# Kernel optimization log

Hardware: AMD Instinct MI355X
Metric: run time of the kernel (lower is better)

## Reference

```python
import jax, jax.numpy as jnp
import numpy as np

T, N, U, K, P = 4096, 256, 128, 32, 128


def setup_inputs() -> dict:
    key = jax.random.key(0)
    ks = jax.random.split(key, 8)
    input_sequence = jax.random.normal(ks[0], (T, U, K), jnp.float32)
    # Stable diagonal dynamics: |A| in (0.5, 0.99), random phase.
    r = jax.random.uniform(ks[1], (N, K), jnp.float32, 0.5, 0.99)
    theta = jax.random.uniform(ks[2], (N, K), jnp.float32, 0.0, np.pi)
    A_re = r * jnp.cos(theta)
    A_im = r * jnp.sin(theta)
    s_b = 1.0 / np.sqrt(U)
    s_c = 1.0 / np.sqrt(N)
    B_re = jax.random.normal(ks[3], (N, U), jnp.float32) * s_b
    B_im = jax.random.normal(ks[4], (N, U), jnp.float32) * s_b
    C_re = jax.random.normal(ks[5], (P, N), jnp.float32) * s_c
    C_im = jax.random.normal(ks[6], (P, N), jnp.float32) * s_c
    D = jax.random.normal(ks[7], (P, U), jnp.float32) * s_b
    return dict(input_sequence=input_sequence, A_re=A_re, A_im=A_im,
                B_re=B_re, B_im=B_im, C_re=C_re, C_im=C_im, D=D)


def _binary_op(elem_i, elem_j):
    # (a_i, s_i) o (a_j, s_j) = (a_i * a_j, a_j * s_i + s_j)
    a_i, s_i = elem_i
    a_j, s_j = elem_j
    return (a_i * a_j, a_j * s_i + s_j)


def reference(input_sequence, A_re, A_im, B_re, B_im, C_re, C_im, D):
    A = (A_re + 1j * A_im).astype(jnp.complex64)        # (N, K) diagonal
    Bm = (B_re + 1j * B_im).astype(jnp.complex64)        # (N, U)
    Cm = (C_re + 1j * C_im).astype(jnp.complex64)        # (P, N)
    x_c = input_sequence.astype(jnp.complex64)           # (T, U, K)
    # inputs_t = B @ x_t  -> (T, N, K)
    inputs = jnp.einsum('nu,tuk->tnk', Bm, x_c)
    systems = jnp.broadcast_to(A, (input_sequence.shape[0],) + A.shape)
    _, states = jax.lax.associative_scan(_binary_op, (systems, inputs))
    # out_t = C @ state_t -> (T, P, K)
    out = jnp.real(jnp.einsum('pn,tnk->tpk', Cm, states))
    Du = jnp.einsum('pu,tuk->tpk', D, input_sequence)    # 2D D branch
    return out + Du
```

## Files before the change

kernel.cpp:

```cpp
#include <hip/hip_runtime.h>
#include <hip/hip_bf16.h>

namespace {

constexpr int T = 4096, N = 256, U = 128, K = 32, P = 128;
constexpr int NK = N * K;
constexpr int CL = 16;
constexpr int NCH = T / CL;
constexpr int NG = NCH / 8;
constexpr int TB = 8;

typedef __attribute__((ext_vector_type(8))) short short8;
typedef __attribute__((ext_vector_type(4))) float f32x4;
typedef __attribute__((address_space(3))) unsigned lds_u32;
typedef __attribute__((address_space(1))) const unsigned glb_u32;

__device__ __forceinline__ unsigned short f2bf(float f) {
  union { float f; unsigned u; } v; v.f = f;
  unsigned r = v.u + 0x7FFFu + ((v.u >> 16) & 1u);
  return (unsigned short)(r >> 16);
}
__device__ __forceinline__ float bf2f(unsigned short s) {
  union { unsigned u; float f; } v; v.u = ((unsigned)s) << 16;
  return v.f;
}
__device__ __forceinline__ short8 ld8(const unsigned short* p) {
  return *reinterpret_cast<const short8*>(p);
}
__device__ __forceinline__ void dma16(const unsigned* g, unsigned* l) {
  __builtin_amdgcn_global_load_lds((glb_u32*)g, (lds_u32*)l, 16, 0, 0);
}
__device__ __forceinline__ void csq(float& pr, float& pi) {
  float nr = pr * pr - pi * pi, ni = 2.f * pr * pi; pr = nr; pi = ni;
}

__device__ __forceinline__ int zswz(int k, int n) {
  int n8 = n >> 3, j = n & 7;
  return k * 256 + ((n8 ^ (k & 7)) << 3) + (j ^ (((k >> 3) & 1) << 2));
}

__device__ __forceinline__ void unpackAB(uint4 a, uint4 b, short8& re, short8& im) {
  union { short8 v; unsigned u[4]; } r, i;
  r.u[0] = (a.x & 0xFFFFu) | (a.y << 16);
  i.u[0] = (a.x >> 16)     | (a.y & 0xFFFF0000u);
  r.u[1] = (a.z & 0xFFFFu) | (a.w << 16);
  i.u[1] = (a.z >> 16)     | (a.w & 0xFFFF0000u);
  r.u[2] = (b.x & 0xFFFFu) | (b.y << 16);
  i.u[2] = (b.x >> 16)     | (b.y & 0xFFFF0000u);
  r.u[3] = (b.z & 0xFFFFu) | (b.w << 16);
  i.u[3] = (b.z >> 16)     | (b.w & 0xFFFF0000u);
  re = r.v; im = i.v;
}

__global__ __launch_bounds__(256) void k_params(
    const float* Are, const float* Aim, const float* Bre, const float* Bim,
    const float* Cre, const float* Cim, const float* D,
    unsigned short* bre, unsigned short* bim, unsigned short* cre,
    unsigned short* cimn, unsigned short* dbf, float* atre, float* atim) {
  int idx = blockIdx.x * 256 + threadIdx.x;
  int stride = gridDim.x * 256;
  for (int i = idx; i < N * U; i += stride) { bre[i] = f2bf(Bre[i]); bim[i] = f2bf(Bim[i]); }
  for (int i = idx; i < P * N; i += stride) { cre[i] = f2bf(Cre[i]); cimn[i] = f2bf(-Cim[i]); }
  for (int i = idx; i < P * U; i += stride) { dbf[i] = f2bf(D[i]); }
  for (int i = idx; i < NK; i += stride) {
    int k = i >> 8, r = i & 255;
    int n8 = (r >> 3) ^ (k & 7);
    int j  = (r & 7) ^ (((k >> 3) & 1) << 2);
    int n = n8 * 8 + j;
    atre[i] = Are[n * K + k];
    atim[i] = Aim[n * K + k];
  }
}

__global__ __launch_bounds__(256) void k_castx(const float* x, unsigned* xTu) {
  __shared__ float lds[U * 33];
  int t = blockIdx.x, tid = threadIdx.x;
  const float* xt = x + (size_t)t * (U * K);
#pragma unroll
  for (int it = 0; it < 16; it++) {
    int idx = it * 256 + tid;
    int u = idx >> 5, k = idx & 31;
    lds[u * 33 + k] = xt[idx];
  }
  __syncthreads();
  unsigned* dst = xTu + (size_t)t * (K * U / 2);
#pragma unroll
  for (int it = 0; it < 8; it++) {
    int k = it * 4 + (tid >> 6);
    int up = tid & 63;
    float f0 = lds[(2 * up) * 33 + k];
    float f1 = lds[(2 * up + 1) * 33 + k];
    dst[k * 64 + up] = (unsigned)f2bf(f0) | ((unsigned)f2bf(f1) << 16);
  }
}

__global__ __launch_bounds__(256)
__attribute__((amdgpu_waves_per_eu(2, 2)))
void k_bgemm(const unsigned short* xT, const unsigned short* bre,
             const unsigned short* bim, unsigned* zbuf, int t0) {
  int blk = blockIdx.x, tid = threadIdx.x;
  int w = tid >> 6, l = tid & 63, lq = l >> 4, lr = l & 15;
  short8 Bf_re[4][4], Bf_im[4][4];
#pragma unroll
  for (int s = 0; s < 4; s++)
#pragma unroll
    for (int nt = 0; nt < 4; nt++) {
      int n0 = (w * 4 + nt) * 16;
      Bf_re[s][nt] = ld8(bre + (n0 + lr) * U + s * 32 + lq * 8);
      Bf_im[s][nt] = ld8(bim + (n0 + lr) * U + s * 32 + lq * 8);
    }
#pragma unroll
  for (int tl = 0; tl < TB; tl++) {
    int tloc = blk * TB + tl;
    const unsigned short* xrow = xT + (size_t)(t0 + tloc) * (K * U);
    short8 af[4][2];
#pragma unroll
    for (int s = 0; s < 4; s++) {
      af[s][0] = ld8(xrow + lr * U + s * 32 + lq * 8);
      af[s][1] = ld8(xrow + (16 + lr) * U + s * 32 + lq * 8);
    }
    f32x4 accre[2][4], accim[2][4];
#pragma unroll
    for (int a = 0; a < 2; a++)
#pragma unroll
      for (int b = 0; b < 4; b++) { accre[a][b] = (f32x4)0.f; accim[a][b] = (f32x4)0.f; }
#pragma unroll
    for (int s = 0; s < 4; s++)
#pragma unroll
      for (int nt = 0; nt < 4; nt++)
#pragma unroll
        for (int mt = 0; mt < 2; mt++) {
          accre[mt][nt] = __builtin_amdgcn_mfma_f32_16x16x32_bf16(af[s][mt], Bf_re[s][nt], accre[mt][nt], 0, 0, 0);
          accim[mt][nt] = __builtin_amdgcn_mfma_f32_16x16x32_bf16(af[s][mt], Bf_im[s][nt], accim[mt][nt], 0, 0, 0);
        }
    unsigned* dst = zbuf + (size_t)tloc * NK;
#pragma unroll
    for (int mt = 0; mt < 2; mt++)
#pragma unroll
      for (int nt = 0; nt < 4; nt++) {
        int n0 = (w * 4 + nt) * 16;
#pragma unroll
        for (int r = 0; r < 4; r++) {
          int krow = mt * 16 + lq * 4 + r;
          dst[zswz(krow, n0 + lr)] =
              (unsigned)f2bf(accre[mt][nt][r]) | ((unsigned)f2bf(accim[mt][nt][r]) << 16);
        }
      }
  }
}

__global__ __launch_bounds__(256) void k_scanA(const unsigned* zbuf, const float* atre,
                                               const float* atim, float2* cend, int c0) {
  int bid = blockIdx.x;
  int cl = bid >> 5;
  int lane = (bid & 31) * 256 + threadIdx.x;
  float ar = atre[lane], ai = atim[lane];
  float sr = 0.f, si = 0.f;
  const unsigned* src = zbuf + (size_t)cl * CL * NK + lane;
#pragma unroll 8
  for (int i = 0; i < CL; i++) {
    unsigned v = src[(size_t)i * NK];
    float ur = bf2f((unsigned short)(v & 0xFFFFu));
    float ui = bf2f((unsigned short)(v >> 16));
    float nr = ar * sr - ai * si + ur;
    float ni = ar * si + ai * sr + ui;
    sr = nr; si = ni;
  }
  cend[(size_t)(c0 + cl) * NK + lane] = make_float2(sr, si);
}

__global__ __launch_bounds__(256) void k_carryg(const float2* cend, const float* atre,
                                                const float* atim, float2* gagg) {
  int bid = blockIdx.x;
  int g = bid >> 5;
  int lane = (bid & 31) * 256 + threadIdx.x;
  float pr = atre[lane], pi = atim[lane];
#pragma unroll
  for (int i = 0; i < 4; i++) csq(pr, pi);
  float agr = 0.f, agi = 0.f;
#pragma unroll
  for (int j = 0; j < 8; j++) {
    float2 e = cend[(size_t)(g * 8 + j) * NK + lane];
    float nr = pr * agr - pi * agi + e.x;
    float ni = pr * agi + pi * agr + e.y;
    agr = nr; agi = ni;
  }
  gagg[(size_t)g * NK + lane] = make_float2(agr, agi);
}

__global__ __launch_bounds__(256) void k_carryb(float2* gagg, const float* atre,
                                                const float* atim) {
  int lane = blockIdx.x * 256 + threadIdx.x;
  float pr = atre[lane], pi = atim[lane];
#pragma unroll
  for (int i = 0; i < 7; i++) csq(pr, pi);
  float cr = 0.f, ci = 0.f;
  for (int gg = 0; gg < NG / 8; gg++) {
    float2 buf[8];
#pragma unroll
    for (int j = 0; j < 8; j++) buf[j] = gagg[(size_t)(gg * 8 + j) * NK + lane];
#pragma unroll
    for (int j = 0; j < 8; j++) {
      gagg[(size_t)(gg * 8 + j) * NK + lane] = make_float2(cr, ci);
      float nr = pr * cr - pi * ci + buf[j].x;
      float ni = pr * ci + pi * cr + buf[j].y;
      cr = nr; ci = ni;
    }
  }
}

__global__ __launch_bounds__(256) void k_carryf(float2* cend, const float* atre,
                                                const float* atim, const float2* gagg) {
  int bid = blockIdx.x;
  int g = bid >> 5;
  int lane = (bid & 31) * 256 + threadIdx.x;
  float pr = atre[lane], pi = atim[lane];
#pragma unroll
  for (int i = 0; i < 4; i++) csq(pr, pi);
  float2 c = gagg[(size_t)g * NK + lane];
  float cr = c.x, ci = c.y;
#pragma unroll
  for (int j = 0; j < 8; j++) {
    size_t off = (size_t)(g * 8 + j) * NK + lane;
    float2 e = cend[off];
    cend[off] = make_float2(cr, ci);
    float nr = pr * cr - pi * ci + e.x;
    float ni = pr * ci + pi * cr + e.y;
    cr = nr; ci = ni;
  }
}

__global__ __launch_bounds__(512)
__attribute__((amdgpu_waves_per_eu(2, 2)))
void k_scout(const unsigned* zbuf, const float* atre, const float* atim,
             const float2* cend,
             const unsigned short* cre, const unsigned short* cimn,
             const unsigned short* dbf, const unsigned short* xT,
             float* out, int t0, int gc0) {
  __shared__ unsigned ldsz[3][NK];
  int blk = blockIdx.x, tid = threadIdx.x;
  int w = tid >> 6, l = tid & 63, lq = l >> 4, lr = l & 15;
  int h = (lr >> 3) & 1;
  short8 Cf_re[8], Cf_im[8];
#pragma unroll
  for (int s = 0; s < 8; s++) {
    int p = w * 16 + lr;
    Cf_re[s] = ld8(cre  + p * N + s * 32 + lq * 8);
    Cf_im[s] = ld8(cimn + p * N + s * 32 + lq * 8);
  }
  short8 Df[4];
#pragma unroll
  for (int s = 0; s < 4; s++) {
    int p = w * 16 + lr;
    Df[s] = ld8(dbf + p * U + s * 32 + lq * 8);
  }
  float ar[16], ai[16], sr[16], si[16];
  int gc = gc0 + blk;
#pragma unroll
  for (int it = 0; it < 4; it++)
#pragma unroll
    for (int j = 0; j < 4; j++) {
      int idx = it * 2048 + tid * 4 + j;
      int e = it * 4 + j;
      ar[e] = atre[idx]; ai[e] = atim[idx];
      float2 c0 = cend[(size_t)gc * NK + idx];
      sr[e] = c0.x; si[e] = c0.y;
    }
  const unsigned* zch = zbuf + (size_t)(blk * CL) * NK;
#pragma unroll
  for (int it = 0; it < 4; it++)
    dma16(zch + it * 2048 + tid * 4, &ldsz[0][it * 2048 + tid * 4]);
#pragma unroll
  for (int it = 0; it < 4; it++)
    dma16(zch + NK + it * 2048 + tid * 4, &ldsz[1][it * 2048 + tid * 4]);

  int bc = 0;
  for (int tl = 0; tl < CL; tl++) {
    int t = t0 + blk * CL + tl;
    const unsigned short* xt = xT + (size_t)t * (K * U);
    short8 xfr[4][2];
#pragma unroll
    for (int s = 0; s < 4; s++)
#pragma unroll
      for (int kt = 0; kt < 2; kt++)
        xfr[s][kt] = ld8(xt + (kt * 16 + lr) * U + s * 32 + lq * 8);
    if (tl == 0) { asm volatile("s_waitcnt vmcnt(12)" ::: "memory"); }
    else         { asm volatile("s_waitcnt vmcnt(20)" ::: "memory"); }
    unsigned* zl = &ldsz[bc][0];
#pragma unroll
    for (int it = 0; it < 4; it++) {
      unsigned* p4 = zl + it * 2048 + tid * 4;
      uint4 v = *reinterpret_cast<const uint4*>(p4);
      unsigned d0 = v.x, d1 = v.y, d2 = v.z, d3 = v.w;
#pragma unroll
      for (int j = 0; j < 4; j++) {
        unsigned dv = (j == 0) ? d0 : (j == 1) ? d1 : (j == 2) ? d2 : d3;
        int e = it * 4 + j;
        float ur = bf2f((unsigned short)(dv & 0xFFFFu));
        float ui = bf2f((unsigned short)(dv >> 16));
        float nr = ar[e] * sr[e] - ai[e] * si[e] + ur;
        float ni = ar[e] * si[e] + ai[e] * sr[e] + ui;
        sr[e] = nr; si[e] = ni;
        dv = (unsigned)f2bf(nr) | ((unsigned)f2bf(ni) << 16);
        if (j == 0) d0 = dv; else if (j == 1) d1 = dv; else if (j == 2) d2 = dv; else d3 = dv;
      }
      uint4 o; o.x = d0; o.y = d1; o.z = d2; o.w = d3;
      *reinterpret_cast<uint4*>(p4) = o;
    }
    asm volatile("s_waitcnt lgkmcnt(0)" ::: "memory");
    __builtin_amdgcn_s_barrier();
    __builtin_amdgcn_sched_barrier(0);
    if (tl + 2 < CL) {
      int bn = bc + 2; if (bn >= 3) bn -= 3;
      const unsigned* zn = zbuf + (size_t)(blk * CL + tl + 2) * NK;
#pragma unroll
      for (int it = 0; it < 4; it++)
        dma16(zn + it * 2048 + tid * 4, &ldsz[bn][it * 2048 + tid * 4]);
    }
    f32x4 acc[2];
    acc[0] = (f32x4)0.f; acc[1] = (f32x4)0.f;
    const unsigned* zs = &ldsz[bc][0];
#pragma unroll
    for (int s = 0; s < 8; s++) {
      short8 bfr[2], bfi[2];
#pragma unroll
      for (int kt = 0; kt < 2; kt++) {
        int k = kt * 16 + lr;
        int n8 = s * 4 + lq;
        const uint4* qp = reinterpret_cast<const uint4*>(zs + k * 256 + ((n8 ^ (k & 7)) << 3));
        uint4 a = qp[h], b = qp[h ^ 1];
        unpackAB(a, b, bfr[kt], bfi[kt]);
      }
#pragma unroll
      for (int kt = 0; kt < 2; kt++) {
        acc[kt] = __builtin_amdgcn_mfma_f32_16x16x32_bf16(Cf_re[s], bfr[kt], acc[kt], 0, 0, 0);
        acc[kt] = __builtin_amdgcn_mfma_f32_16x16x32_bf16(Cf_im[s], bfi[kt], acc[kt], 0, 0, 0);
      }
    }
#pragma unroll
    for (int s = 0; s < 4; s++)
#pragma unroll
      for (int kt = 0; kt < 2; kt++)
        acc[kt] = __builtin_amdgcn_mfma_f32_16x16x32_bf16(Df[s], xfr[s][kt], acc[kt], 0, 0, 0);
    float* ot = out + (size_t)t * (P * K);
#pragma unroll
    for (int kt = 0; kt < 2; kt++)
#pragma unroll
      for (int r = 0; r < 4; r++) {
        int p = w * 16 + lq * 4 + r;
        int k = kt * 16 + lr;
        ot[p * K + k] = acc[kt][r];
      }
    bc = bc + 1; if (bc >= 3) bc -= 3;
  }
}

}

extern "C" void kernel_launch(void* const* d_in, const int* in_sizes, int n_in,
                              void* d_out, int out_size, void* d_ws, size_t ws_size,
                              hipStream_t stream) {
  const float* x   = (const float*)d_in[0];
  const float* Are = (const float*)d_in[1];
  const float* Aim = (const float*)d_in[2];
  const float* Bre = (const float*)d_in[3];
  const float* Bim = (const float*)d_in[4];
  const float* Cre = (const float*)d_in[5];
  const float* Cim = (const float*)d_in[6];
  const float* D   = (const float*)d_in[7];
  float* out = (float*)d_out;

  auto al = [](size_t x_) { return (x_ + 255) & ~(size_t)255; };
  const size_t fixed = al((size_t)T * K * U * 2)
                     + al((size_t)NCH * NK * 8)
                     + al((size_t)NG * NK * 8)
                     + 2 * al((size_t)N * U * 2)
                     + 2 * al((size_t)P * N * 2)
                     + al((size_t)P * U * 2)
                     + 2 * al((size_t)NK * 4);
  int S = 64;
  for (int s : {1, 2, 4, 8, 16, 32, 64}) {
    if (fixed + al((size_t)(T / s) * NK * 4) <= ws_size) { S = s; break; }
  }
  const int TS = T / S;
  const int CS = NCH / S;

  char* w = (char*)d_ws;
  auto alloc = [&](size_t bytes) { void* p = (void*)w; w += (bytes + 255) & ~(size_t)255; return p; };
  unsigned* zbuf       = (unsigned*)alloc((size_t)TS * NK * 4);
  unsigned* xTu        = (unsigned*)alloc((size_t)T * K * U * 2);
  float2* cend         = (float2*)alloc((size_t)NCH * NK * 8);
  float2* gagg         = (float2*)alloc((size_t)NG * NK * 8);
  unsigned short* bre  = (unsigned short*)alloc((size_t)N * U * 2);
  unsigned short* bim  = (unsigned short*)alloc((size_t)N * U * 2);
  unsigned short* cre  = (unsigned short*)alloc((size_t)P * N * 2);
  unsigned short* cimn = (unsigned short*)alloc((size_t)P * N * 2);
  unsigned short* dbf  = (unsigned short*)alloc((size_t)P * U * 2);
  float* atre          = (float*)alloc((size_t)NK * 4);
  float* atim          = (float*)alloc((size_t)NK * 4);

  k_params<<<64, 256, 0, stream>>>(Are, Aim, Bre, Bim, Cre, Cim, D,
                                   bre, bim, cre, cimn, dbf, atre, atim);
  k_castx<<<T, 256, 0, stream>>>(x, xTu);

  const unsigned short* xT16 = (const unsigned short*)xTu;
  for (int q = 0; q < S; q++) {
    k_bgemm<<<TS / TB, 256, 0, stream>>>(xT16, bre, bim, zbuf, q * TS);
    k_scanA<<<CS * 32, 256, 0, stream>>>(zbuf, atre, atim, cend, q * CS);
  }
  k_carryg<<<NG * 32, 256, 0, stream>>>(cend, atre, atim, gagg);
  k_carryb<<<NK / 256, 256, 0, stream>>>(gagg, atre, atim);
  k_carryf<<<NG * 32, 256, 0, stream>>>(cend, atre, atim, gagg);
  for (int q = 0; q < S; q++) {
    if (S > 1)
      k_bgemm<<<TS / TB, 256, 0, stream>>>(xT16, bre, bim, zbuf, q * TS);
    k_scout<<<TS / CL, 512, 0, stream>>>(zbuf, atre, atim, cend,
                                         cre, cimn, dbf, xT16, out, q * TS, q * CS);
  }
}
```

Before: 265.8 us.

## Fuse chunk-local scan into B-GEMM kernel and drop separate scan pass

```diff
diff --git a/kernel.cpp b/kernel.cpp
--- a/kernel.cpp
+++ b/kernel.cpp
@@ -8,7 +8,7 @@
 constexpr int CL = 16;
 constexpr int NCH = T / CL;
 constexpr int NG = NCH / 8;
-constexpr int TB = 8;
+constexpr int TB = 16;
 
 typedef __attribute__((ext_vector_type(8))) short short8;
 typedef __attribute__((ext_vector_type(4))) float f32x4;
@@ -94,21 +94,36 @@
   }
 }
 
-__global__ __launch_bounds__(256)
+__global__ __launch_bounds__(512)
 __attribute__((amdgpu_waves_per_eu(2, 2)))
 void k_bgemm(const unsigned short* xT, const unsigned short* bre,
-             const unsigned short* bim, unsigned* zbuf, int t0) {
+             const unsigned short* bim, const float* atre, const float* atim,
+             unsigned* zbuf, float2* cend, int t0, int c0, int wr_cend) {
   int blk = blockIdx.x, tid = threadIdx.x;
   int w = tid >> 6, l = tid & 63, lq = l >> 4, lr = l & 15;
-  short8 Bf_re[4][4], Bf_im[4][4];
+  short8 Bf_re[4][2], Bf_im[4][2];
 #pragma unroll
   for (int s = 0; s < 4; s++)
 #pragma unroll
-    for (int nt = 0; nt < 4; nt++) {
-      int n0 = (w * 4 + nt) * 16;
+    for (int nt = 0; nt < 2; nt++) {
+      int n0 = (w * 2 + nt) * 16;
       Bf_re[s][nt] = ld8(bre + (n0 + lr) * U + s * 32 + lq * 8);
       Bf_im[s][nt] = ld8(bim + (n0 + lr) * U + s * 32 + lq * 8);
     }
+  float ar[16], ai[16], sr[16], si[16];
+#pragma unroll
+  for (int mt = 0; mt < 2; mt++)
+#pragma unroll
+    for (int nt = 0; nt < 2; nt++)
+#pragma unroll
+      for (int r = 0; r < 4; r++) {
+        int e = mt * 8 + nt * 4 + r;
+        int krow = mt * 16 + lq * 4 + r;
+        int n = (w * 2 + nt) * 16 + lr;
+        int idx = zswz(krow, n);
+        ar[e] = atre[idx]; ai[e] = atim[idx];
+        sr[e] = 0.f; si[e] = 0.f;
+      }
 #pragma unroll
   for (int tl = 0; tl < TB; tl++) {
     int tloc = blk * TB + tl;
@@ -119,15 +134,15 @@
       af[s][0] = ld8(xrow + lr * U + s * 32 + lq * 8);
       af[s][1] = ld8(xrow + (16 + lr) * U + s * 32 + lq * 8);
     }
-    f32x4 accre[2][4], accim[2][4];
+    f32x4 accre[2][2], accim[2][2];
 #pragma unroll
     for (int a = 0; a < 2; a++)
 #pragma unroll
-      for (int b = 0; b < 4; b++) { accre[a][b] = (f32x4)0.f; accim[a][b] = (f32x4)0.f; }
+      for (int b = 0; b < 2; b++) { accre[a][b] = (f32x4)0.f; accim[a][b] = (f32x4)0.f; }
 #pragma unroll
     for (int s = 0; s < 4; s++)
 #pragma unroll
-      for (int nt = 0; nt < 4; nt++)
+      for (int nt = 0; nt < 2; nt++)
 #pragma unroll
         for (int mt = 0; mt < 2; mt++) {
           accre[mt][nt] = __builtin_amdgcn_mfma_f32_16x16x32_bf16(af[s][mt], Bf_re[s][nt], accre[mt][nt], 0, 0, 0);
@@ -137,36 +152,37 @@
 #pragma unroll
     for (int mt = 0; mt < 2; mt++)
 #pragma unroll
-      for (int nt = 0; nt < 4; nt++) {
-        int n0 = (w * 4 + nt) * 16;
+      for (int nt = 0; nt < 2; nt++) {
+        int n0 = (w * 2 + nt) * 16;
 #pragma unroll
         for (int r = 0; r < 4; r++) {
           int krow = mt * 16 + lq * 4 + r;
-          dst[zswz(krow, n0 + lr)] =
-              (unsigned)f2bf(accre[mt][nt][r]) | ((unsigned)f2bf(accim[mt][nt][r]) << 16);
+          unsigned dv = (unsigned)f2bf(accre[mt][nt][r]) |
+                        ((unsigned)f2bf(accim[mt][nt][r]) << 16);
+          dst[zswz(krow, n0 + lr)] = dv;
+          int e = mt * 8 + nt * 4 + r;
+          float ur = bf2f((unsigned short)(dv & 0xFFFFu));
+          float ui = bf2f((unsigned short)(dv >> 16));
+          float nr2 = ar[e] * sr[e] - ai[e] * si[e] + ur;
+          float ni2 = ar[e] * si[e] + ai[e] * sr[e] + ui;
+          sr[e] = nr2; si[e] = ni2;
         }
       }
   }
-}
-
-__global__ __launch_bounds__(256) void k_scanA(const unsigned* zbuf, const float* atre,
-                                               const float* atim, float2* cend, int c0) {
-  int bid = blockIdx.x;
-  int cl = bid >> 5;
-  int lane = (bid & 31) * 256 + threadIdx.x;
-  float ar = atre[lane], ai = atim[lane];
-  float sr = 0.f, si = 0.f;
-  const unsigned* src = zbuf + (size_t)cl * CL * NK + lane;
-#pragma unroll 8
-  for (int i = 0; i < CL; i++) {
-    unsigned v = src[(size_t)i * NK];
-    float ur = bf2f((unsigned short)(v & 0xFFFFu));
-    float ui = bf2f((unsigned short)(v >> 16));
-    float nr = ar * sr - ai * si + ur;
-    float ni = ar * si + ai * sr + ui;
-    sr = nr; si = ni;
-  }
-  cend[(size_t)(c0 + cl) * NK + lane] = make_float2(sr, si);
+  if (wr_cend) {
+    float2* ce = cend + (size_t)(c0 + blk) * NK;
+#pragma unroll
+    for (int mt = 0; mt < 2; mt++)
+#pragma unroll
+      for (int nt = 0; nt < 2; nt++)
+#pragma unroll
+        for (int r = 0; r < 4; r++) {
+          int e = mt * 8 + nt * 4 + r;
+          int krow = mt * 16 + lq * 4 + r;
+          int n = (w * 2 + nt) * 16 + lr;
+          ce[zswz(krow, n)] = make_float2(sr[e], si[e]);
+        }
+  }
 }
 
 __global__ __launch_bounds__(256) void k_carryg(const float2* cend, const float* atre,
@@ -404,16 +420,16 @@
   k_castx<<<T, 256, 0, stream>>>(x, xTu);
 
   const unsigned short* xT16 = (const unsigned short*)xTu;
-  for (int q = 0; q < S; q++) {
-    k_bgemm<<<TS / TB, 256, 0, stream>>>(xT16, bre, bim, zbuf, q * TS);
-    k_scanA<<<CS * 32, 256, 0, stream>>>(zbuf, atre, atim, cend, q * CS);
-  }
+  for (int q = 0; q < S; q++)
+    k_bgemm<<<TS / TB, 512, 0, stream>>>(xT16, bre, bim, atre, atim,
+                                         zbuf, cend, q * TS, q * CS, 1);
   k_carryg<<<NG * 32, 256, 0, stream>>>(cend, atre, atim, gagg);
   k_carryb<<<NK / 256, 256, 0, stream>>>(gagg, atre, atim);
   k_carryf<<<NG * 32, 256, 0, stream>>>(cend, atre, atim, gagg);
   for (int q = 0; q < S; q++) {
     if (S > 1)
-      k_bgemm<<<TS / TB, 256, 0, stream>>>(xT16, bre, bim, zbuf, q * TS);
+      k_bgemm<<<TS / TB, 512, 0, stream>>>(xT16, bre, bim, atre, atim,
+                                           zbuf, cend, q * TS, q * CS, 0);
     k_scout<<<TS / CL, 512, 0, stream>>>(zbuf, atre, atim, cend,
                                          cre, cimn, dbf, xT16, out, q * TS, q * CS);
   }
```

Result: slower. 480.6 us (+80.8%).
